# Kernel optimization log

Measured on AMD Instinct MI355X. Metric: run time of the kernel, lower is better.

## Reference

```python
import jax, jax.numpy as jnp
import numpy as np

DIM = 1024
HEADS = 16
HIDDEN = 4096
EPS = 1e-5

def setup_inputs() -> dict:
    key = jax.random.key(0)
    ks = jax.random.split(key, 8)
    s = 0.02
    return {
        "x": jax.random.normal(ks[0], (4, 1024, DIM), dtype=jnp.float32),
        "ln1_g": jnp.ones((DIM,), jnp.float32),
        "ln1_b": jnp.zeros((DIM,), jnp.float32),
        "w_qkv": jax.random.normal(ks[1], (DIM, 3 * DIM), jnp.float32) * s,
        "b_qkv": jnp.zeros((3 * DIM,), jnp.float32),
        "w_proj": jax.random.normal(ks[2], (DIM, DIM), jnp.float32) * s,
        "b_proj": jnp.zeros((DIM,), jnp.float32),
        "ln2_g": jnp.ones((DIM,), jnp.float32),
        "ln2_b": jnp.zeros((DIM,), jnp.float32),
        "w_fc1": jax.random.normal(ks[3], (DIM, HIDDEN), jnp.float32) * s,
        "b_fc1": jnp.zeros((HIDDEN,), jnp.float32),
        "w_fc2": jax.random.normal(ks[4], (HIDDEN, DIM), jnp.float32) * s,
        "b_fc2": jnp.zeros((DIM,), jnp.float32),
    }

def _layernorm(x, g, b):
    mu = jnp.mean(x, axis=-1, keepdims=True)
    var = jnp.mean(jnp.square(x - mu), axis=-1, keepdims=True)
    return (x - mu) * jax.lax.rsqrt(var + EPS) * g + b

def _block(x, ln1_g, ln1_b, w_qkv, b_qkv, w_proj, b_proj,
           ln2_g, ln2_b, w_fc1, b_fc1, w_fc2, b_fc2):
    B, N, C = x.shape
    H = HEADS
    Dh = C // H
    scale = Dh ** -0.5
    # --- attention branch (pre-norm) ---
    h = _layernorm(x, ln1_g, ln1_b)
    qkv = h @ w_qkv + b_qkv                       # [B,N,3C]
    qkv = qkv.reshape(B, N, 3, H, Dh)
    q, k, v = qkv[:, :, 0], qkv[:, :, 1], qkv[:, :, 2]  # [B,N,H,Dh]
    attn = jnp.einsum("bnhd,bmhd->bhnm", q, k) * scale  # [B,H,N,N]
    attn = jax.nn.softmax(attn, axis=-1)
    o = jnp.einsum("bhnm,bmhd->bnhd", attn, v).reshape(B, N, C)
    x = x + (o @ w_proj + b_proj)
    # --- MLP branch (pre-norm) ---
    h = _layernorm(x, ln2_g, ln2_b)
    h = jax.nn.gelu(h @ w_fc1 + b_fc1, approximate=False)
    x = x + (h @ w_fc2 + b_fc2)
    return x

def reference(x, ln1_g, ln1_b, w_qkv, b_qkv, w_proj, b_proj,
              ln2_g, ln2_b, w_fc1, b_fc1, w_fc2, b_fc2):
    return _block(x, ln1_g, ln1_b, w_qkv, b_qkv, w_proj, b_proj,
                  ln2_g, ln2_b, w_fc1, b_fc1, w_fc2, b_fc2)
```

## Files before the change

kernel.cpp:

```cpp
#include <hip/hip_runtime.h>
#include <hip/hip_bf16.h>

typedef __attribute__((ext_vector_type(8))) short bf16x8;
typedef __attribute__((ext_vector_type(4))) float f32x4;

__device__ __forceinline__ ushort f2bf(float f) {
  unsigned int u = __float_as_uint(f);
  u += 0x7fffu + ((u >> 16) & 1u);
  return (ushort)(u >> 16);
}

__device__ __forceinline__ void gl_lds16(const void* g, void* l) {
  __builtin_amdgcn_global_load_lds(
      (const __attribute__((address_space(1))) void*)g,
      (__attribute__((address_space(3))) void*)l, 16, 0, 0);
}

#define SB() __builtin_amdgcn_sched_barrier(0)

__global__ __launch_bounds__(256) void transpose_w(
    const float* __restrict__ W, ushort* __restrict__ Wt, int K, int N) {
  __shared__ float tile[32][33];
  const int tx = threadIdx.x, ty = threadIdx.y;
  const int bx = blockIdx.x, by = blockIdx.y;
#pragma unroll
  for (int j = 0; j < 4; j++)
    tile[ty + j * 8][tx] = W[(size_t)(by * 32 + ty + j * 8) * N + bx * 32 + tx];
  __syncthreads();
#pragma unroll
  for (int j = 0; j < 4; j++)
    Wt[(size_t)(bx * 32 + ty + j * 8) * K + by * 32 + tx] =
        f2bf(tile[tx][ty + j * 8]);
}

__global__ __launch_bounds__(256) void transpose_v(
    const ushort* __restrict__ qkv, ushort* __restrict__ vt) {
  __shared__ ushort tile[32][33];
  const int tx = threadIdx.x, ty = threadIdx.y;
  const int n0 = blockIdx.x * 32;
  const int d0 = blockIdx.y * 32;
  const int bh = blockIdx.z;
  const int bidx = bh >> 4, h = bh & 15;
#pragma unroll
  for (int j = 0; j < 4; j++)
    tile[ty + j * 8][tx] =
        qkv[(size_t)(bidx * 1024 + n0 + ty + j * 8) * 3072 + 2048 + h * 64 +
            d0 + tx];
  __syncthreads();
#pragma unroll
  for (int j = 0; j < 4; j++)
    vt[(size_t)(bh * 64 + d0 + ty + j * 8) * 1024 + n0 + tx] =
        tile[tx][ty + j * 8];
}

__global__ __launch_bounds__(256) void ln_bf16(
    const float* __restrict__ x, const float* __restrict__ g,
    const float* __restrict__ b, ushort* __restrict__ out) {
  const int row = blockIdx.x;
  const int t = threadIdx.x;
  float4 v = ((const float4*)(x + (size_t)row * 1024))[t];
  float s = v.x + v.y + v.z + v.w;
  float ss = v.x * v.x + v.y * v.y + v.z * v.z + v.w * v.w;
#pragma unroll
  for (int msk = 1; msk < 64; msk <<= 1) {
    s += __shfl_xor(s, msk);
    ss += __shfl_xor(ss, msk);
  }
  __shared__ float red[8];
  const int wv = t >> 6, ln = t & 63;
  if (ln == 0) { red[wv * 2] = s; red[wv * 2 + 1] = ss; }
  __syncthreads();
  s = red[0] + red[2] + red[4] + red[6];
  ss = red[1] + red[3] + red[5] + red[7];
  const float mu = s * (1.0f / 1024.0f);
  const float var = ss * (1.0f / 1024.0f) - mu * mu;
  const float rstd = rsqrtf(var + 1e-5f);
  float4 gv = ((const float4*)g)[t];
  float4 bv = ((const float4*)b)[t];
  ushort4 o;
  o.x = f2bf((v.x - mu) * rstd * gv.x + bv.x);
  o.y = f2bf((v.y - mu) * rstd * gv.y + bv.y);
  o.z = f2bf((v.z - mu) * rstd * gv.z + bv.z);
  o.w = f2bf((v.w - mu) * rstd * gv.w + bv.w);
  ((ushort4*)(out + (size_t)row * 1024))[t] = o;
}

template <int BM, int BN, int NW, int OCC, int EPI>
__global__ __launch_bounds__(NW * 64, OCC) void gemm2ph(
    const ushort* __restrict__ A, const ushort* __restrict__ Bt,
    const float* __restrict__ bias, const float* __restrict__ resid,
    void* __restrict__ outp, int M, int N, int K, int cw, int ch, int xw) {
  constexpr int WN = NW / 2;
  constexpr int BWN = BN / WN;
  constexpr int MF = BM / 2 / 16;
  constexpr int NF = BWN / 16;
  constexpr int CA = BM / 64, CB = BN / 64;
  __shared__ ushort smem[2 * (BM + BN) * 32];
  const int t = threadIdx.x;
  const int lane = t & 63, wid = t >> 6;
  const int lr = lane & 15, lc = lane >> 4;
  const int wr = wid / WN, wc = wid % WN;

  const int flat = blockIdx.y * gridDim.x + blockIdx.x;
  const int xcd = flat & 7, li = flat >> 3;
  const int bx = (xcd % xw) * cw + (li % cw);
  const int by = (xcd / xw) * ch + (li / cw);
  const int m0 = by * BM, n0 = bx * BN;
  const int nkt = K >> 5;

  const int uoff = ((t & 3) ^ ((t >> 3) & 3)) * 8;
  const int au = (lc ^ ((lr >> 1) & 3)) * 8;

  f32x4 acc[MF][NF];
#pragma unroll
  for (int m = 0; m < MF; m++)
#pragma unroll
    for (int n = 0; n < NF; n++) acc[m][n] = (f32x4){0.f, 0.f, 0.f, 0.f};

  auto stage = [&](int bb, int kt) {
#pragma unroll
    for (int c = 0; c < CA; c++)
      gl_lds16(A + (size_t)(m0 + c * 64 + (t >> 2)) * K + (size_t)(kt * 32) +
                   uoff,
               &smem[bb * BM * 32 + c * 2048 + wid * 512]);
#pragma unroll
    for (int c = 0; c < CB; c++)
      gl_lds16(Bt + (size_t)(n0 + c * 64 + (t >> 2)) * K + (size_t)(kt * 32) +
                   uoff,
               &smem[2 * BM * 32 + bb * BN * 32 + c * 2048 + wid * 512]);
  };
  auto rdA = [&](int bb, int mf) {
    return *(const bf16x8*)&smem[bb * BM * 32 +
                                 (wr * (BM / 2) + mf * 16 + lr) * 32 + au];
  };
  auto rdB = [&](int bb, int nf) {
    return *(const bf16x8*)&smem[2 * BM * 32 + bb * BN * 32 +
                                 (wc * BWN + nf * 16 + lr) * 32 + au];
  };

  stage(0, 0);
  asm volatile("s_waitcnt vmcnt(0)" ::: "memory");
  SB(); __builtin_amdgcn_s_barrier(); SB();

  int b = 0;
  for (int kt = 0; kt < nkt; kt++, b ^= 1) {
    if (kt + 1 < nkt) stage(b ^ 1, kt + 1);

    bf16x8 Br[NF];
#pragma unroll
    for (int nf = 0; nf < NF; nf++) Br[nf] = rdB(b, nf);
    bf16x8 Ar[MF];
#pragma unroll
    for (int mf = 0; mf < MF; mf++) Ar[mf] = rdA(b, mf);
    __builtin_amdgcn_s_setprio(1);
#pragma unroll
    for (int mf = 0; mf < MF; mf++)
#pragma unroll
      for (int nf = 0; nf < NF; nf++)
        acc[mf][nf] = __builtin_amdgcn_mfma_f32_16x16x32_bf16(
            Ar[mf], Br[nf], acc[mf][nf], 0, 0, 0);
    __builtin_amdgcn_s_setprio(0);

    asm volatile("s_waitcnt vmcnt(0)" ::: "memory");
    SB(); __builtin_amdgcn_s_barrier(); SB();
  }

#pragma unroll
  for (int mf = 0; mf < MF; mf++) {
#pragma unroll
    for (int nf = 0; nf < NF; nf++) {
      const int gr0 = m0 + wr * (BM / 2) + mf * 16 + lc * 4;
      const int gc = n0 + wc * BWN + nf * 16 + lr;
      const float bs = bias[gc];
#pragma unroll
      for (int r = 0; r < 4; r++) {
        const float v = acc[mf][nf][r] + bs;
        const int gr = gr0 + r;
        if (EPI == 0) {
          ((ushort*)outp)[(size_t)gr * N + gc] = f2bf(v);
        } else if (EPI == 1) {
          const float gg = 0.5f * v * (1.0f + erff(v * 0.70710678118654752f));
          ((ushort*)outp)[(size_t)gr * N + gc] = f2bf(gg);
        } else {
          ((float*)outp)[(size_t)gr * N + gc] =
              v + resid[(size_t)gr * N + gc];
        }
      }
    }
  }
}

__global__ __launch_bounds__(256) void attn_kernel(
    const ushort* __restrict__ qkv, const ushort* __restrict__ vt,
    ushort* __restrict__ o_out) {
  __shared__ ushort sK[4096];
  __shared__ ushort sV[4096];
  __shared__ ushort sP[4 * 32 * 72];
  const int t = threadIdx.x;
  const int lane = t & 63, wid = t >> 6;
  const int lr = lane & 15, lc = lane >> 4;
  const int qb = blockIdx.x;
  const int bh = blockIdx.y;
  const int bidx = bh >> 4, h = bh & 15;
  const size_t base = (size_t)bidx * 1024 * 3072;
  const int q0w = qb * 128 + wid * 32;

  bf16x8 qf[2][2];
#pragma unroll
  for (int nf = 0; nf < 2; nf++)
#pragma unroll
    for (int kd = 0; kd < 2; kd++)
      qf[nf][kd] = *(const bf16x8*)&qkv[base +
          (size_t)(q0w + nf * 16 + lr) * 3072 + h * 64 + kd * 32 + lc * 8];

  f32x4 oacc[4][2];
#pragma unroll
  for (int mf = 0; mf < 4; mf++)
#pragma unroll
    for (int nf = 0; nf < 2; nf++) oacc[mf][nf] = (f32x4){0.f, 0.f, 0.f, 0.f};
  float m_r[2] = {-1e30f, -1e30f};
  float l_r[2] = {0.f, 0.f};

  const int srow = lane >> 2;
  const int scol = (lane & 3) * 8;
  ushort* pw = sP + wid * 2304;

  for (int kv0 = 0; kv0 < 1024; kv0 += 64) {
    __syncthreads();
#pragma unroll
    for (int s = 0; s < 2; s++) {
      gl_lds16(qkv + base + (size_t)(kv0 + wid * 16 + srow) * 3072 + 1024 +
                   h * 64 + s * 32 + scol,
               sK + s * 2048 + wid * 512);
      gl_lds16(vt + (size_t)(bh * 64 + wid * 16 + srow) * 1024 + kv0 + s * 32 +
                   scol,
               sV + s * 2048 + wid * 512);
    }
    __syncthreads();

    f32x4 st[4][2];
#pragma unroll
    for (int mf = 0; mf < 4; mf++) {
      bf16x8 ka0 = *(const bf16x8*)&sK[(mf * 16 + lr) * 32 + lc * 8];
      bf16x8 ka1 = *(const bf16x8*)&sK[2048 + (mf * 16 + lr) * 32 + lc * 8];
#pragma unroll
      for (int nf = 0; nf < 2; nf++) {
        f32x4 z = (f32x4){0.f, 0.f, 0.f, 0.f};
        z = __builtin_amdgcn_mfma_f32_16x16x32_bf16(ka0, qf[nf][0], z, 0, 0, 0);
        z = __builtin_amdgcn_mfma_f32_16x16x32_bf16(ka1, qf[nf][1], z, 0, 0, 0);
        st[mf][nf] = z;
      }
    }

#pragma unroll
    for (int nf = 0; nf < 2; nf++) {
      float mx = st[0][nf][0];
#pragma unroll
      for (int mf = 0; mf < 4; mf++)
        mx = fmaxf(mx, fmaxf(fmaxf(st[mf][nf][0], st[mf][nf][1]),
                             fmaxf(st[mf][nf][2], st[mf][nf][3])));
      mx = fmaxf(mx, __shfl_xor(mx, 16));
      mx = fmaxf(mx, __shfl_xor(mx, 32));
      mx *= 0.125f;
      const float mn = fmaxf(m_r[nf], mx);
      const float alpha = __expf(m_r[nf] - mn);
      m_r[nf] = mn;
      float rs = 0.f;
#pragma unroll
      for (int mf = 0; mf < 4; mf++) {
        const float p0 = __expf(fmaf(st[mf][nf][0], 0.125f, -mn));
        const float p1 = __expf(fmaf(st[mf][nf][1], 0.125f, -mn));
        const float p2 = __expf(fmaf(st[mf][nf][2], 0.125f, -mn));
        const float p3 = __expf(fmaf(st[mf][nf][3], 0.125f, -mn));
        rs += (p0 + p1) + (p2 + p3);
        uint2 u;
        u.x = (uint)f2bf(p0) | ((uint)f2bf(p1) << 16);
        u.y = (uint)f2bf(p2) | ((uint)f2bf(p3) << 16);
        *(uint2*)&pw[(nf * 16 + lr) * 72 + mf * 16 + lc * 4] = u;
      }
      rs += __shfl_xor(rs, 16);
      rs += __shfl_xor(rs, 32);
      l_r[nf] = l_r[nf] * alpha + rs;
#pragma unroll
      for (int mf = 0; mf < 4; mf++) {
        oacc[mf][nf][0] *= alpha;
        oacc[mf][nf][1] *= alpha;
        oacc[mf][nf][2] *= alpha;
        oacc[mf][nf][3] *= alpha;
      }
    }

#pragma unroll
    for (int ks = 0; ks < 2; ks++) {
      bf16x8 pb0 = *(const bf16x8*)&pw[lr * 72 + ks * 32 + lc * 8];
      bf16x8 pb1 = *(const bf16x8*)&pw[(16 + lr) * 72 + ks * 32 + lc * 8];
#pragma unroll
      for (int mf = 0; mf < 4; mf++) {
        bf16x8 va = *(const bf16x8*)&sV[ks * 2048 + (mf * 16 + lr) * 32 + lc * 8];
        oacc[mf][0] =
            __builtin_amdgcn_mfma_f32_16x16x32_bf16(va, pb0, oacc[mf][0], 0, 0, 0);
        oacc[mf][1] =
            __builtin_amdgcn_mfma_f32_16x16x32_bf16(va, pb1, oacc[mf][1], 0, 0, 0);
      }
    }
  }

  const float inv[2] = {1.f / l_r[0], 1.f / l_r[1]};
#pragma unroll
  for (int mf = 0; mf < 4; mf++)
#pragma unroll
    for (int nf = 0; nf < 2; nf++) {
      ushort4 o4;
      o4.x = f2bf(oacc[mf][nf][0] * inv[nf]);
      o4.y = f2bf(oacc[mf][nf][1] * inv[nf]);
      o4.z = f2bf(oacc[mf][nf][2] * inv[nf]);
      o4.w = f2bf(oacc[mf][nf][3] * inv[nf]);
      *(ushort4*)&o_out[(size_t)(bidx * 1024 + q0w + nf * 16 + lr) * 1024 +
                        h * 64 + mf * 16 + lc * 4] = o4;
    }
}

extern "C" void kernel_launch(void* const* d_in, const int* in_sizes, int n_in,
                              void* d_out, int out_size, void* d_ws,
                              size_t ws_size, hipStream_t stream) {
  const float* x      = (const float*)d_in[0];
  const float* ln1_g  = (const float*)d_in[1];
  const float* ln1_b  = (const float*)d_in[2];
  const float* w_qkv  = (const float*)d_in[3];
  const float* b_qkv  = (const float*)d_in[4];
  const float* w_proj = (const float*)d_in[5];
  const float* b_proj = (const float*)d_in[6];
  const float* ln2_g  = (const float*)d_in[7];
  const float* ln2_b  = (const float*)d_in[8];
  const float* w_fc1  = (const float*)d_in[9];
  const float* b_fc1  = (const float*)d_in[10];
  const float* w_fc2  = (const float*)d_in[11];
  const float* b_fc2  = (const float*)d_in[12];
  float* out = (float*)d_out;

  ushort* ws      = (ushort*)d_ws;
  ushort* wt_qkv  = ws;
  ushort* wt_proj = wt_qkv + 3072 * 1024;
  ushort* wt_fc1  = wt_proj + 1024 * 1024;
  ushort* wt_fc2  = wt_fc1 + 4096 * 1024;
  ushort* hbuf    = wt_fc2 + 1024 * 4096;
  ushort* qkv     = hbuf + 4096 * 1024;
  ushort* obuf    = qkv + 4096 * 3072;
  ushort* h3      = qkv;
  ushort* vtb     = hbuf;

  transpose_w<<<dim3(96, 32), dim3(32, 8), 0, stream>>>(w_qkv, wt_qkv, 1024, 3072);
  transpose_w<<<dim3(32, 32), dim3(32, 8), 0, stream>>>(w_proj, wt_proj, 1024, 1024);
  transpose_w<<<dim3(128, 32), dim3(32, 8), 0, stream>>>(w_fc1, wt_fc1, 1024, 4096);
  transpose_w<<<dim3(32, 128), dim3(32, 8), 0, stream>>>(w_fc2, wt_fc2, 4096, 1024);

  ln_bf16<<<4096, 256, 0, stream>>>(x, ln1_g, ln1_b, hbuf);
  gemm2ph<128, 128, 4, 4, 0><<<dim3(24, 32), 256, 0, stream>>>(
      hbuf, wt_qkv, b_qkv, nullptr, qkv, 4096, 3072, 1024, 12, 8, 2);
  transpose_v<<<dim3(32, 2, 64), dim3(32, 8), 0, stream>>>(qkv, vtb);
  attn_kernel<<<dim3(8, 64), 256, 0, stream>>>(qkv, vtb, obuf);
  gemm2ph<128, 64, 4, 4, 2><<<dim3(16, 32), 256, 0, stream>>>(
      obuf, wt_proj, b_proj, x, out, 4096, 1024, 1024, 8, 8, 2);
  ln_bf16<<<4096, 256, 0, stream>>>(out, ln2_g, ln2_b, hbuf);
  gemm2ph<128, 128, 4, 4, 1><<<dim3(32, 32), 256, 0, stream>>>(
      hbuf, wt_fc1, b_fc1, nullptr, h3, 4096, 4096, 1024, 16, 8, 2);
  gemm2ph<128, 64, 4, 4, 2><<<dim3(16, 32), 256, 0, stream>>>(
      h3, wt_fc2, b_fc2, out, out, 4096, 1024, 4096, 8, 8, 2);
}
```

Measured before the change: 245.4 us.

## Triple-buffer GEMM LDS staging with two-tile-ahead prefetch and partial vmcnt waits

Converts the double-buffered GEMM main loop to a three-buffer ring. Global-to-LDS loads are issued two K-tiles ahead, and the loop waits only for the older outstanding stage using partial vmcnt counts. This is meant to hide more global memory latency behind MFMA work. LDS use grows by half, and the occupancy hint for the 128x128 GEMMs drops from 4 to 3.

Result: no change. 241.6 us (-1.5%).

```diff
diff --git a/kernel.cpp b/kernel.cpp
--- a/kernel.cpp
+++ b/kernel.cpp
@@ -86,7 +86,7 @@
 }
 
 template <int BM, int BN, int NW, int OCC, int EPI>
-__global__ __launch_bounds__(NW * 64, OCC) void gemm2ph(
+__global__ __launch_bounds__(NW * 64, OCC) void gemm3b(
     const ushort* __restrict__ A, const ushort* __restrict__ Bt,
     const float* __restrict__ bias, const float* __restrict__ resid,
     void* __restrict__ outp, int M, int N, int K, int cw, int ch, int xw) {
@@ -95,7 +95,8 @@
   constexpr int MF = BM / 2 / 16;
   constexpr int NF = BWN / 16;
   constexpr int CA = BM / 64, CB = BN / 64;
-  __shared__ ushort smem[2 * (BM + BN) * 32];
+  constexpr int SC = CA + CB;
+  __shared__ ushort smem[3 * (BM + BN) * 32];
   const int t = threadIdx.x;
   const int lane = t & 63, wid = t >> 6;
   const int lr = lane & 15, lc = lane >> 4;
@@ -127,31 +128,39 @@
     for (int c = 0; c < CB; c++)
       gl_lds16(Bt + (size_t)(n0 + c * 64 + (t >> 2)) * K + (size_t)(kt * 32) +
                    uoff,
-               &smem[2 * BM * 32 + bb * BN * 32 + c * 2048 + wid * 512]);
+               &smem[3 * BM * 32 + bb * BN * 32 + c * 2048 + wid * 512]);
   };
   auto rdA = [&](int bb, int mf) {
     return *(const bf16x8*)&smem[bb * BM * 32 +
                                  (wr * (BM / 2) + mf * 16 + lr) * 32 + au];
   };
   auto rdB = [&](int bb, int nf) {
-    return *(const bf16x8*)&smem[2 * BM * 32 + bb * BN * 32 +
+    return *(const bf16x8*)&smem[3 * BM * 32 + bb * BN * 32 +
                                  (wc * BWN + nf * 16 + lr) * 32 + au];
   };
 
   stage(0, 0);
-  asm volatile("s_waitcnt vmcnt(0)" ::: "memory");
+  if (nkt > 1) {
+    stage(1, 1);
+    if constexpr (SC == 4) asm volatile("s_waitcnt vmcnt(4)" ::: "memory");
+    else                   asm volatile("s_waitcnt vmcnt(3)" ::: "memory");
+  } else {
+    asm volatile("s_waitcnt vmcnt(0)" ::: "memory");
+  }
   SB(); __builtin_amdgcn_s_barrier(); SB();
 
-  int b = 0;
-  for (int kt = 0; kt < nkt; kt++, b ^= 1) {
-    if (kt + 1 < nkt) stage(b ^ 1, kt + 1);
+  int rb = 0;
+  for (int kt = 0; kt < nkt; kt++) {
+    const int sb = (rb >= 1) ? rb - 1 : 2;
+    const bool pf = (kt + 2 < nkt);
+    if (pf) stage(sb, kt + 2);
 
     bf16x8 Br[NF];
 #pragma unroll
-    for (int nf = 0; nf < NF; nf++) Br[nf] = rdB(b, nf);
+    for (int nf = 0; nf < NF; nf++) Br[nf] = rdB(rb, nf);
     bf16x8 Ar[MF];
 #pragma unroll
-    for (int mf = 0; mf < MF; mf++) Ar[mf] = rdA(b, mf);
+    for (int mf = 0; mf < MF; mf++) Ar[mf] = rdA(rb, mf);
     __builtin_amdgcn_s_setprio(1);
 #pragma unroll
     for (int mf = 0; mf < MF; mf++)
@@ -161,8 +170,14 @@
             Ar[mf], Br[nf], acc[mf][nf], 0, 0, 0);
     __builtin_amdgcn_s_setprio(0);
 
-    asm volatile("s_waitcnt vmcnt(0)" ::: "memory");
+    if (pf) {
+      if constexpr (SC == 4) asm volatile("s_waitcnt vmcnt(4)" ::: "memory");
+      else                   asm volatile("s_waitcnt vmcnt(3)" ::: "memory");
+    } else {
+      asm volatile("s_waitcnt vmcnt(0)" ::: "memory");
+    }
     SB(); __builtin_amdgcn_s_barrier(); SB();
+    rb = (rb == 2) ? 0 : rb + 1;
   }
 
 #pragma unroll
@@ -355,15 +370,15 @@
   transpose_w<<<dim3(32, 128), dim3(32, 8), 0, stream>>>(w_fc2, wt_fc2, 4096, 1024);
 
   ln_bf16<<<4096, 256, 0, stream>>>(x, ln1_g, ln1_b, hbuf);
-  gemm2ph<128, 128, 4, 4, 0><<<dim3(24, 32), 256, 0, stream>>>(
+  gemm3b<128, 128, 4, 3, 0><<<dim3(24, 32), 256, 0, stream>>>(
       hbuf, wt_qkv, b_qkv, nullptr, qkv, 4096, 3072, 1024, 12, 8, 2);
   transpose_v<<<dim3(32, 2, 64), dim3(32, 8), 0, stream>>>(qkv, vtb);
   attn_kernel<<<dim3(8, 64), 256, 0, stream>>>(qkv, vtb, obuf);
-  gemm2ph<128, 64, 4, 4, 2><<<dim3(16, 32), 256, 0, stream>>>(
+  gemm3b<128, 64, 4, 4, 2><<<dim3(16, 32), 256, 0, stream>>>(
       obuf, wt_proj, b_proj, x, out, 4096, 1024, 1024, 8, 8, 2);
   ln_bf16<<<4096, 256, 0, stream>>>(out, ln2_g, ln2_b, hbuf);
-  gemm2ph<128, 128, 4, 4, 1><<<dim3(32, 32), 256, 0, stream>>>(
+  gemm3b<128, 128, 4, 3, 1><<<dim3(32, 32), 256, 0, stream>>>(
       hbuf, wt_fc1, b_fc1, nullptr, h3, 4096, 4096, 1024, 16, 8, 2);
-  gemm2ph<128, 64, 4, 4, 2><<<dim3(16, 32), 256, 0, stream>>>(
+  gemm3b<128, 64, 4, 4, 2><<<dim3(16, 32), 256, 0, stream>>>(
       h3, wt_fc2, b_fc2, out, out, 4096, 1024, 4096, 8, 8, 2);
 }
```
